# Performance work log

Hardware: AMD Instinct MI355X
Metric: run time of the kernel (lower is better)

The kernel has to match this reference:

```python
import jax, jax.numpy as jnp
import numpy as np

D_MODEL = 1024
H = 16
D_K = D_MODEL // H


def setup_inputs() -> dict:
    key = jax.random.key(0)
    ks = jax.random.split(key, 9)
    s = 0.02
    x = jax.random.normal(ks[0], (2, 2048, D_MODEL), dtype=jnp.float32)
    Wq = jax.random.normal(ks[1], (D_MODEL, D_MODEL), dtype=jnp.float32) * s
    bq = jax.random.normal(ks[2], (D_MODEL,), dtype=jnp.float32) * s
    Wk = jax.random.normal(ks[3], (D_MODEL, D_MODEL), dtype=jnp.float32) * s
    bk = jax.random.normal(ks[4], (D_MODEL,), dtype=jnp.float32) * s
    Wv = jax.random.normal(ks[5], (D_MODEL, D_MODEL), dtype=jnp.float32) * s
    bv = jax.random.normal(ks[6], (D_MODEL,), dtype=jnp.float32) * s
    Wo = jax.random.normal(ks[7], (D_MODEL, D_MODEL), dtype=jnp.float32) * s
    bo = jax.random.normal(ks[8], (D_MODEL,), dtype=jnp.float32) * s
    return {"x": x, "Wq": Wq, "bq": bq, "Wk": Wk, "bk": bk,
            "Wv": Wv, "bv": bv, "Wo": Wo, "bo": bo}


def reference(x, Wq, bq, Wk, bk, Wv, bv, Wo, bo):
    b, s, _ = x.shape
    scale = 1.0 / jnp.sqrt(jnp.float32(D_K))
    # projections; [b, s, d] -> [b, h, s, d_k]
    def split_heads(t):
        return t.reshape(b, s, H, D_K).transpose(0, 2, 1, 3)
    q = split_heads(x @ Wq + bq)
    k = split_heads(x @ Wk + bk)
    v = split_heads(x @ Wv + bv)
    scores = jnp.einsum('bhqd,bhkd->bhqk', q, k) * scale  # [b,h,s,s]
    attn = jax.nn.softmax(scores, axis=-1)
    ctx = jnp.einsum('bhqk,bhkd->bhqd', attn, v)
    ctx = ctx.transpose(0, 2, 1, 3).reshape(b, s, D_MODEL)
    return ctx @ Wo + bo + x
```

## Files before the change

### kernel.cpp

```cpp
#include <hip/hip_runtime.h>
#include <hip/hip_bf16.h>
#include <stdint.h>

#define D_MODEL 1024
#define NH 16
#define DK 64
#define S_LEN 2048

typedef __attribute__((ext_vector_type(8))) __bf16 bf16x8;
typedef __attribute__((ext_vector_type(4))) float f32x4;

#define GLOBAL_AS __attribute__((address_space(1)))
#define LDS_AS    __attribute__((address_space(3)))

__device__ __forceinline__ void async16(const ushort* g, ushort* l) {
    __builtin_amdgcn_global_load_lds(
        (const GLOBAL_AS uint32_t*)(uintptr_t)(const void*)g,
        (LDS_AS uint32_t*)(uint32_t)(uintptr_t)(void*)l,
        16, 0, 0);
}

template <int N>
__device__ __forceinline__ void pipe_barrier() {
    asm volatile("s_waitcnt vmcnt(%0)\n\ts_barrier" :: "n"(N) : "memory");
}

__device__ __forceinline__ float fast_exp2(float x) {
    float r;
    asm("v_exp_f32 %0, %1" : "=v"(r) : "v"(x));
    return r;
}

__device__ __forceinline__ ushort f2bf(float f) {
    union { float f; uint32_t u; } v; v.f = f;
    uint32_t lsb = (v.u >> 16) & 1u;
    return (ushort)((v.u + 0x7fffu + lsb) >> 16);
}

__device__ __forceinline__ uint32_t packbf(float a, float b) {
    union { float f; uint32_t u; } x, y; x.f = a; y.f = b;
    return ((x.u + 0x8000u) >> 16) | ((y.u + 0x8000u) & 0xffff0000u);
}

__device__ __forceinline__ uint32_t packbf_rn(float a, float b) {
    union { __hip_bfloat162 h; uint32_t u; } cv;
    cv.h = __float22bfloat162_rn(make_float2(a, b));
    return cv.u;
}

__device__ __forceinline__ bf16x8 ldfrag(const ushort* p) {
    union { uint4 u; bf16x8 b; } cv;
    cv.u = *(const uint4*)p;
    return cv.b;
}


__global__ void cvt_x_kernel(const float* __restrict__ x, ushort* __restrict__ xb) {
    int i = blockIdx.x * 256 + threadIdx.x;
    float4 v = ((const float4*)x)[i];
    ushort4 o;
    o.x = f2bf(v.x); o.y = f2bf(v.y); o.z = f2bf(v.z); o.w = f2bf(v.w);
    ((ushort4*)xb)[i] = o;
}

__global__ void transpose_cvt4_kernel(
    const float* __restrict__ W0, const float* __restrict__ W1,
    const float* __restrict__ W2, const float* __restrict__ W3,
    ushort* __restrict__ D0, ushort* __restrict__ D1,
    ushort* __restrict__ D2, ushort* __restrict__ D3) {
    const float* W; ushort* D;
    switch (blockIdx.z) {
        case 0: W = W0; D = D0; break;
        case 1: W = W1; D = D1; break;
        case 2: W = W2; D = D2; break;
        default: W = W3; D = D3; break;
    }
    __shared__ float tile[32][33];
    int bx = blockIdx.x * 32, by = blockIdx.y * 32;
    int tx = threadIdx.x, ty = threadIdx.y;
#pragma unroll
    for (int j = 0; j < 32; j += 8)
        tile[ty + j][tx] = W[(size_t)(by + ty + j) * D_MODEL + bx + tx];
    __syncthreads();
#pragma unroll
    for (int j = 0; j < 32; j += 8)
        D[(size_t)(bx + ty + j) * D_MODEL + by + tx] = f2bf(tile[tx][ty + j]);
}

__global__ void cvt_bias_kernel(const float* __restrict__ bq, const float* __restrict__ bk,
                                const float* __restrict__ bv, float* __restrict__ out) {
    int i = blockIdx.x * 256 + threadIdx.x;
    float v = (i < 1024) ? bq[i] : (i < 2048 ? bk[i - 1024] : bv[i - 2048]);
    out[i] = v;
}

template <int MODE>
__global__ __launch_bounds__(256, 3) void gemm_kernel(
    const ushort* __restrict__ A, const ushort* __restrict__ Bt,
    const float* __restrict__ bias,
    ushort* __restrict__ outQ, ushort* __restrict__ outK, ushort* __restrict__ outVt,
    const float* __restrict__ xres, float* __restrict__ outF) {
    constexpr int BN = (MODE == 0) ? 128 : 64;
    constexpr int NI = (MODE == 0) ? 4 : 2;
    constexpr int NS = (MODE == 0) ? 4 : 3;
    constexpr int ABUF = 4096;
    constexpr int BBUF = (MODE == 0) ? 4096 : 2048;
    constexpr int SMEM = (MODE == 0) ? 24576 : 18432;
    __shared__ __align__(16) ushort smem[SMEM];
    ushort* sAb = smem;
    ushort* sBb = smem + 3 * ABUF;

    const int tid = threadIdx.x;
    const int wave = tid >> 6, lane = tid & 63;
    const int lr = lane & 15, lq = lane >> 4;
    const int srow = lane >> 3, sp = lane & 7;

    const int bid = blockIdx.x;
    const int xcd = bid & 7, lb = bid >> 3;
    int bx, by;
    if (MODE == 0) { bx = xcd * 3 + (lb % 3); by = lb / 3; }
    else           { by = xcd * 4 + (lb & 3); bx = lb >> 2; }
    const int blockM = by * 128;
    const int blockN = bx * BN;
    const int waveM = (wave >> 1) * 64;
    const int waveN = (MODE == 0) ? (wave & 1) * 64 : (wave & 1) * 32;

    auto stage = [&](int k0, int buf) {
        ushort* a = sAb + buf * ABUF;
#pragma unroll
        for (int t = 0; t < 2; t++) {
            int Rb = wave * 16 + t * 8;
            int R = Rb + srow;
            int L = sp ^ (R & 7);
            int m = 2 * R + (L >> 2);
            int kc = L & 3;
            async16(&A[(size_t)(blockM + m) * D_MODEL + k0 + kc * 8], a + Rb * 64);
        }
        ushort* b = sBb + buf * BBUF;
        if (MODE == 0) {
#pragma unroll
            for (int t = 0; t < 2; t++) {
                int Rb = wave * 16 + t * 8;
                int R = Rb + srow;
                int L = sp ^ (R & 7);
                int n = 2 * R + (L >> 2);
                int kc = L & 3;
                async16(&Bt[(size_t)(blockN + n) * D_MODEL + k0 + kc * 8], b + Rb * 64);
            }
        } else {
            int Rb = wave * 8;
            int R = Rb + srow;
            int L = sp ^ (R & 7);
            int n = 2 * R + (L >> 2);
            int kc = L & 3;
            async16(&Bt[(size_t)(blockN + n) * D_MODEL + k0 + kc * 8], b + Rb * 64);
        }
    };

    const int RA = (waveM >> 1) + (lr >> 1);
    const int offA = RA * 64 + ((((lr & 1) * 4 + lq) ^ (RA & 7)) * 8);
    const int RB = (waveN >> 1) + (lr >> 1);
    const int offB = RB * 64 + ((((lr & 1) * 4 + lq) ^ (RB & 7)) * 8);

    f32x4 acc[4][NI] = {};

    stage(0, 0);
    stage(32, 1);
    pipe_barrier<NS>();

#pragma unroll
    for (int k = 0; k < 32; k++) {
        const int buf = k % 3;
        if (k + 2 < 32) stage((k + 2) * 32, (k + 2) % 3);
        const ushort* a = sAb + buf * ABUF;
        const ushort* b = sBb + buf * BBUF;
        bf16x8 af[4], bfr[NI];
#pragma unroll
        for (int mi = 0; mi < 4; mi++)
            af[mi] = ldfrag(&a[offA + mi * 512]);
#pragma unroll
        for (int ni = 0; ni < NI; ni++)
            bfr[ni] = ldfrag(&b[offB + ni * 512]);
#pragma unroll
        for (int mi = 0; mi < 4; mi++)
#pragma unroll
            for (int ni = 0; ni < NI; ni++)
                acc[mi][ni] = __builtin_amdgcn_mfma_f32_16x16x32_bf16(
                    af[mi], bfr[ni], acc[mi][ni], 0, 0, 0);
        if (k < 30) pipe_barrier<NS>();
        else if (k == 30) pipe_barrier<0>();
    }
    __syncthreads();

    const int bglob = blockM >> 11;
    const int sbase = blockM & 2047;

    if (MODE == 0) {
        const int which = bx >> 3;
        if (which < 2) {
            const float scale = (which == 0) ? 0.1803368801f : 1.0f;
#pragma unroll
            for (int ni = 0; ni < 4; ni++) {
                const int n_loc = waveN + ni * 16 + lr;
                const float bn = bias[blockN + n_loc];
#pragma unroll
                for (int mi = 0; mi < 4; mi++)
#pragma unroll
                    for (int r = 0; r < 4; r++) {
                        int m_loc = waveM + mi * 16 + lq * 4 + r;
                        smem[m_loc * 136 + n_loc] =
                            f2bf((acc[mi][ni][r] + bn) * scale);
                    }
            }
            __syncthreads();
            ushort* outp = (which == 0) ? outQ : outK;
            const int hbase = (which == 0) ? bx * 2 : (bx - 8) * 2;
#pragma unroll
            for (int j = 0; j < 8; j++) {
                int c = tid + j * 256;
                int m = c >> 4, nc = c & 15;
                int hh = nc >> 3, d8 = nc & 7;
                uint4 w = *(uint4*)&smem[m * 136 + nc * 8];
                size_t bh = (size_t)(bglob * NH + hbase + hh);
                *(uint4*)&outp[(bh * S_LEN + sbase + m) * DK + d8 * 8] = w;
            }
        } else {
#pragma unroll
            for (int ni = 0; ni < 4; ni++) {
                const int n_loc = waveN + ni * 16 + lr;
                const float bn = bias[blockN + n_loc];
#pragma unroll
                for (int mi = 0; mi < 4; mi++) {
                    uint2 w;
                    w.x = packbf(acc[mi][ni][0] + bn, acc[mi][ni][1] + bn);
                    w.y = packbf(acc[mi][ni][2] + bn, acc[mi][ni][3] + bn);
                    int m_base = waveM + mi * 16 + lq * 4;
                    *(uint2*)&smem[n_loc * 136 + m_base] = w;
                }
            }
            __syncthreads();
            const int hbase = (bx - 16) * 2;
#pragma unroll
            for (int j = 0; j < 8; j++) {
                int c = tid + j * 256;
                int n_loc = c >> 4, m8 = c & 15;
                int d = n_loc & 63, hh = n_loc >> 6;
                uint4 w = *(uint4*)&smem[n_loc * 136 + m8 * 8];
                size_t bh = (size_t)(bglob * NH + hbase + hh);
                *(uint4*)&outVt[(bh * DK + d) * S_LEN + sbase + m8 * 8] = w;
            }
        }
    } else {
        float* sCf = (float*)smem;
#pragma unroll
        for (int ni = 0; ni < 2; ni++) {
            const int n_loc = waveN + ni * 16 + lr;
            const float bn = bias[blockN + n_loc];
#pragma unroll
            for (int mi = 0; mi < 4; mi++)
#pragma unroll
                for (int r = 0; r < 4; r++) {
                    int m_loc = waveM + mi * 16 + lq * 4 + r;
                    sCf[m_loc * 68 + n_loc] = acc[mi][ni][r] + bn;
                }
        }
        __syncthreads();
#pragma unroll
        for (int j = 0; j < 8; j++) {
            int c = tid + j * 256;
            int m = c >> 4, nc = c & 15;
            float4 v = *(float4*)&sCf[m * 68 + nc * 4];
            size_t idx = (size_t)(blockM + m) * D_MODEL + blockN + nc * 4;
            float4 xr = *(const float4*)&xres[idx];
            v.x += xr.x; v.y += xr.y; v.z += xr.z; v.w += xr.w;
            *(float4*)&outF[idx] = v;
        }
    }
}

__global__ __launch_bounds__(256, 3) void attn_kernel(
    const ushort* __restrict__ Q, const ushort* __restrict__ Km,
    const ushort* __restrict__ Vt, ushort* __restrict__ ctx) {
    const int bid = blockIdx.x;
    const int xcd = bid & 7, lb = bid >> 3;
    const int bh = xcd * 4 + (lb & 3);
    const int qt = lb >> 2;
    const int q0 = qt * 128;
    __shared__ __align__(16) ushort sK[2][64 * 64];
    __shared__ __align__(16) ushort sV[2][64 * 64];
    __shared__ __align__(16) ushort sQP[4][32 * 64];
    const int tid = threadIdx.x;
    const int wave = tid >> 6, lane = tid & 63;
    const int lr = lane & 15, lq = lane >> 4;
    const int srow = lane >> 3, sp = lane & 7;
    const ushort* Qh = Q + (size_t)bh * S_LEN * DK;
    const ushort* Kh = Km + (size_t)bh * S_LEN * DK;
    const ushort* Vh = Vt + (size_t)bh * DK * S_LEN;
    ushort* sPw = sQP[wave];

#pragma unroll
    for (int t = 0; t < 4; t++) {
        int row = t * 8 + srow;
        int c = sp ^ (row & 7);
        async16(&Qh[(size_t)(q0 + wave * 32 + row) * DK + c * 8],
                &sPw[t * 8 * 64]);
    }

    auto stageK = [&](int k0, int buf) {
#pragma unroll
        for (int t = 0; t < 2; t++) {
            int row = wave * 16 + t * 8 + srow;
            int c = sp ^ (row & 7);
            async16(&Kh[(size_t)(k0 + row) * DK + c * 8],
                    &sK[buf][(wave * 16 + t * 8) * 64]);
        }
    };
    auto stageV = [&](int k0, int buf) {
#pragma unroll
        for (int t = 0; t < 2; t++) {
            int row = wave * 16 + t * 8 + srow;
            int c = sp ^ (row & 7);
            async16(&Vh[(size_t)row * S_LEN + k0 + c * 8],
                    &sV[buf][(wave * 16 + t * 8) * 64]);
        }
    };

    stageK(0, 0);
    stageV(0, 0);
    stageK(64, 1);
    __syncthreads();

    bf16x8 qf[2][2];
#pragma unroll
    for (int nj = 0; nj < 2; nj++)
#pragma unroll
        for (int kk = 0; kk < 2; kk++)
            qf[nj][kk] = ldfrag(&sPw[(nj * 16 + lr) * 64 +
                                     (((kk * 4 + lq) ^ (lr & 7)) * 8)]);

    union { uint4 u; bf16x8 b; } one_u;
    one_u.u = make_uint4(0x3F803F80u, 0x3F803F80u, 0x3F803F80u, 0x3F803F80u);
    const bf16x8 ones = one_u.b;

    f32x4 cacc[2][4] = {};
    f32x4 ssum[2] = {};

    auto qk = [&](const ushort* sk, f32x4 (*sacc)[2]) {
#pragma unroll
        for (int kk = 0; kk < 2; kk++) {
            bf16x8 kf[4];
            int swz = ((kk * 4 + lq) ^ (lr & 7)) * 8;
#pragma unroll
            for (int mi = 0; mi < 4; mi++)
                kf[mi] = ldfrag(&sk[(mi * 16 + lr) * 64 + swz]);
            __builtin_amdgcn_s_setprio(1);
#pragma unroll
            for (int mi = 0; mi < 4; mi++)
#pragma unroll
                for (int nj = 0; nj < 2; nj++)
                    sacc[mi][nj] = __builtin_amdgcn_mfma_f32_16x16x32_bf16(
                        kf[mi], qf[nj][kk], sacc[mi][nj], 0, 0, 0);
            __builtin_amdgcn_s_setprio(0);
        }
    };

    auto expP = [&](f32x4 (*sacc)[2]) {
#pragma unroll
        for (int mi = 0; mi < 4; mi++)
#pragma unroll
            for (int nj = 0; nj < 2; nj++) {
                float p0 = fast_exp2(sacc[mi][nj][0]);
                float p1 = fast_exp2(sacc[mi][nj][1]);
                float p2 = fast_exp2(sacc[mi][nj][2]);
                float p3 = fast_exp2(sacc[mi][nj][3]);
                uint2 w;
                w.x = packbf_rn(p0, p1);
                w.y = packbf_rn(p2, p3);
                int physc = (mi * 2 + (lq >> 1)) ^ (lr & 7);
                *(uint2*)&sPw[(nj * 16 + lr) * 64 + physc * 8 + (lq & 1) * 4] = w;
            }
    };

    auto pv = [&](const ushort* sv) {
#pragma unroll
        for (int ks = 0; ks < 2; ks++) {
            bf16x8 pf[2], vf[4];
            int swz = ((ks * 4 + lq) ^ (lr & 7)) * 8;
#pragma unroll
            for (int nj = 0; nj < 2; nj++)
                pf[nj] = ldfrag(&sPw[(nj * 16 + lr) * 64 + swz]);
#pragma unroll
            for (int nd = 0; nd < 4; nd++)
                vf[nd] = ldfrag(&sv[(nd * 16 + lr) * 64 + swz]);
            __builtin_amdgcn_s_setprio(1);
#pragma unroll
            for (int nj = 0; nj < 2; nj++)
#pragma unroll
                for (int nd = 0; nd < 4; nd++)
                    cacc[nj][nd] = __builtin_amdgcn_mfma_f32_16x16x32_bf16(
                        pf[nj], vf[nd], cacc[nj][nd], 0, 0, 0);
#pragma unroll
            for (int nj = 0; nj < 2; nj++)
                ssum[nj] = __builtin_amdgcn_mfma_f32_16x16x32_bf16(
                    pf[nj], ones, ssum[nj], 0, 0, 0);
            __builtin_amdgcn_s_setprio(0);
        }
    };

    {
        f32x4 s0[4][2] = {};
        qk(sK[0], s0);
        expP(s0);
    }
    __builtin_amdgcn_s_barrier();

#pragma unroll 2
    for (int k = 0; k < 31; k++) {
        if (k + 2 < 32) stageK((k + 2) * 64, k & 1);
        stageV((k + 1) * 64, (k + 1) & 1);
        f32x4 s2[4][2] = {};
        qk(sK[(k + 1) & 1], s2);
        pv(sV[k & 1]);
        pipe_barrier<0>();
        expP(s2);
    }
    pv(sV[1]);

    const int b = bh >> 4, h = bh & 15;
    float inv[2][4];
#pragma unroll
    for (int nj = 0; nj < 2; nj++)
#pragma unroll
        for (int r = 0; r < 4; r++)
            inv[nj][r] = __builtin_amdgcn_rcpf(ssum[nj][r]);
#pragma unroll
    for (int nj = 0; nj < 2; nj++)
#pragma unroll
        for (int nd = 0; nd < 4; nd++)
#pragma unroll
            for (int r = 0; r < 4; r++) {
                int qrow = q0 + wave * 32 + nj * 16 + lq * 4 + r;
                int d = nd * 16 + lr;
                float v = cacc[nj][nd][r] * inv[nj][r];
                ctx[(size_t)(b * S_LEN + qrow) * D_MODEL + h * DK + d] = f2bf(v);
            }
}


extern "C" void kernel_launch(void* const* d_in, const int* in_sizes, int n_in,
                              void* d_out, int out_size, void* d_ws, size_t ws_size,
                              hipStream_t stream) {
    const float* x  = (const float*)d_in[0];
    const float* Wq = (const float*)d_in[1];
    const float* bq = (const float*)d_in[2];
    const float* Wk = (const float*)d_in[3];
    const float* bk = (const float*)d_in[4];
    const float* Wv = (const float*)d_in[5];
    const float* bv = (const float*)d_in[6];
    const float* Wo = (const float*)d_in[7];
    const float* bo = (const float*)d_in[8];

    char* ws = (char*)d_ws;
    ushort* xb    = (ushort*)(ws);
    ushort* wqkv  = (ushort*)(ws + (8ull  << 20));
    ushort* wo_t  = (ushort*)(ws + (14ull << 20));
    ushort* qbuf  = (ushort*)(ws + (16ull << 20));
    ushort* kbuf  = (ushort*)(ws + (24ull << 20));
    ushort* vtb   = (ushort*)(ws + (32ull << 20));
    ushort* ctx   = (ushort*)(ws + (40ull << 20));
    float*  biasq = (float*)(ws + (48ull << 20));

    cvt_x_kernel<<<4096, 256, 0, stream>>>(x, xb);
    transpose_cvt4_kernel<<<dim3(32, 32, 4), dim3(32, 8), 0, stream>>>(
        Wq, Wk, Wv, Wo, wqkv, wqkv + 1024 * 1024, wqkv + 2 * 1024 * 1024, wo_t);
    cvt_bias_kernel<<<12, 256, 0, stream>>>(bq, bk, bv, biasq);

    gemm_kernel<0><<<768, 256, 0, stream>>>(
        xb, wqkv, biasq, qbuf, kbuf, vtb, nullptr, nullptr);
    attn_kernel<<<512, 256, 0, stream>>>(qbuf, kbuf, vtb, ctx);
    gemm_kernel<1><<<512, 256, 0, stream>>>(
        ctx, wo_t, bo, nullptr, nullptr, nullptr, x, (float*)d_out);
}
```

Measured before the change: 188.5 us.

## Triple-buffer K/V in attention and fuse the three conversion kernels into one launch

The attention kernel moves from double to triple buffering of the K and V LDS tiles. It prefetches one tile further ahead and waits on a partial vmcnt instead of draining all loads each iteration, so global loads overlap more with MFMA work. LDS use grows and launch bounds drop from 3 to 2 blocks per CU, which may lower occupancy. Separately, the x-cast, weight-transpose and bias-copy kernels are merged into a single launch to save two kernel launches.

```diff
diff --git a/kernel.cpp b/kernel.cpp
--- a/kernel.cpp
+++ b/kernel.cpp
@@ -54,44 +54,46 @@
     return cv.b;
 }
 
-
-__global__ void cvt_x_kernel(const float* __restrict__ x, ushort* __restrict__ xb) {
-    int i = blockIdx.x * 256 + threadIdx.x;
-    float4 v = ((const float4*)x)[i];
-    ushort4 o;
-    o.x = f2bf(v.x); o.y = f2bf(v.y); o.z = f2bf(v.z); o.w = f2bf(v.w);
-    ((ushort4*)xb)[i] = o;
-}
-
-__global__ void transpose_cvt4_kernel(
+__global__ void cvt_fused_kernel(
+    const float* __restrict__ x, ushort* __restrict__ xb,
     const float* __restrict__ W0, const float* __restrict__ W1,
     const float* __restrict__ W2, const float* __restrict__ W3,
     ushort* __restrict__ D0, ushort* __restrict__ D1,
-    ushort* __restrict__ D2, ushort* __restrict__ D3) {
-    const float* W; ushort* D;
-    switch (blockIdx.z) {
-        case 0: W = W0; D = D0; break;
-        case 1: W = W1; D = D1; break;
-        case 2: W = W2; D = D2; break;
-        default: W = W3; D = D3; break;
-    }
+    ushort* __restrict__ D2, ushort* __restrict__ D3,
+    const float* __restrict__ bq, const float* __restrict__ bk,
+    const float* __restrict__ bv, float* __restrict__ biasq) {
     __shared__ float tile[32][33];
-    int bx = blockIdx.x * 32, by = blockIdx.y * 32;
-    int tx = threadIdx.x, ty = threadIdx.y;
-#pragma unroll
-    for (int j = 0; j < 32; j += 8)
-        tile[ty + j][tx] = W[(size_t)(by + ty + j) * D_MODEL + bx + tx];
-    __syncthreads();
-#pragma unroll
-    for (int j = 0; j < 32; j += 8)
-        D[(size_t)(bx + ty + j) * D_MODEL + by + tx] = f2bf(tile[tx][ty + j]);
-}
-
-__global__ void cvt_bias_kernel(const float* __restrict__ bq, const float* __restrict__ bk,
-                                const float* __restrict__ bv, float* __restrict__ out) {
-    int i = blockIdx.x * 256 + threadIdx.x;
-    float v = (i < 1024) ? bq[i] : (i < 2048 ? bk[i - 1024] : bv[i - 2048]);
-    out[i] = v;
+    const int bid = blockIdx.x, tid = threadIdx.x;
+    if (bid < 4096) {
+        int i = bid * 256 + tid;
+        float4 v = ((const float4*)x)[i];
+        ushort4 o;
+        o.x = f2bf(v.x); o.y = f2bf(v.y); o.z = f2bf(v.z); o.w = f2bf(v.w);
+        ((ushort4*)xb)[i] = o;
+    } else if (bid < 8192) {
+        int t = bid - 4096;
+        int z = t >> 10, rem = t & 1023;
+        const float* W; ushort* D;
+        switch (z) {
+            case 0: W = W0; D = D0; break;
+            case 1: W = W1; D = D1; break;
+            case 2: W = W2; D = D2; break;
+            default: W = W3; D = D3; break;
+        }
+        int by = (rem >> 5) * 32, bx = (rem & 31) * 32;
+        int tx = tid & 31, ty = tid >> 5;
+#pragma unroll
+        for (int j = 0; j < 32; j += 8)
+            tile[ty + j][tx] = W[(size_t)(by + ty + j) * D_MODEL + bx + tx];
+        __syncthreads();
+#pragma unroll
+        for (int j = 0; j < 32; j += 8)
+            D[(size_t)(bx + ty + j) * D_MODEL + by + tx] = f2bf(tile[tx][ty + j]);
+    } else {
+        int i = (bid - 8192) * 256 + tid;
+        float v = (i < 1024) ? bq[i] : (i < 2048 ? bk[i - 1024] : bv[i - 2048]);
+        biasq[i] = v;
+    }
 }
 
 template <int MODE>
@@ -278,7 +280,7 @@
     }
 }
 
-__global__ __launch_bounds__(256, 3) void attn_kernel(
+__global__ __launch_bounds__(256, 2) void attn_kernel(
     const ushort* __restrict__ Q, const ushort* __restrict__ Km,
     const ushort* __restrict__ Vt, ushort* __restrict__ ctx) {
     const int bid = blockIdx.x;
@@ -286,8 +288,8 @@
     const int bh = xcd * 4 + (lb & 3);
     const int qt = lb >> 2;
     const int q0 = qt * 128;
-    __shared__ __align__(16) ushort sK[2][64 * 64];
-    __shared__ __align__(16) ushort sV[2][64 * 64];
+    __shared__ __align__(16) ushort sK[3][64 * 64];
+    __shared__ __align__(16) ushort sV[3][64 * 64];
     __shared__ __align__(16) ushort sQP[4][32 * 64];
     const int tid = threadIdx.x;
     const int wave = tid >> 6, lane = tid & 63;
@@ -328,6 +330,8 @@
     stageK(0, 0);
     stageV(0, 0);
     stageK(64, 1);
+    stageV(64, 1);
+    stageK(128, 2);
     __syncthreads();
 
     bf16x8 qf[2][2];
@@ -414,17 +418,19 @@
     }
     __builtin_amdgcn_s_barrier();
 
-#pragma unroll 2
+#pragma unroll 3
     for (int k = 0; k < 31; k++) {
-        if (k + 2 < 32) stageK((k + 2) * 64, k & 1);
-        stageV((k + 1) * 64, (k + 1) & 1);
+        if (k + 3 < 32) stageK((k + 3) * 64, (k + 3) % 3);
+        if (k + 2 < 32) stageV((k + 2) * 64, (k + 2) % 3);
         f32x4 s2[4][2] = {};
-        qk(sK[(k + 1) & 1], s2);
-        pv(sV[k & 1]);
-        pipe_barrier<0>();
+        qk(sK[(k + 1) % 3], s2);
+        pv(sV[k % 3]);
+        if (k < 29) pipe_barrier<4>();
+        else if (k == 29) pipe_barrier<2>();
+        else pipe_barrier<0>();
         expP(s2);
     }
-    pv(sV[1]);
+    pv(sV[31 % 3]);
 
     const int b = bh >> 4, h = bh & 15;
     float inv[2][4];
@@ -470,10 +476,10 @@
     ushort* ctx   = (ushort*)(ws + (40ull << 20));
     float*  biasq = (float*)(ws + (48ull << 20));
 
-    cvt_x_kernel<<<4096, 256, 0, stream>>>(x, xb);
-    transpose_cvt4_kernel<<<dim3(32, 32, 4), dim3(32, 8), 0, stream>>>(
-        Wq, Wk, Wv, Wo, wqkv, wqkv + 1024 * 1024, wqkv + 2 * 1024 * 1024, wo_t);
-    cvt_bias_kernel<<<12, 256, 0, stream>>>(bq, bk, bv, biasq);
+    cvt_fused_kernel<<<8204, 256, 0, stream>>>(
+        x, xb, Wq, Wk, Wv, Wo,
+        wqkv, wqkv + 1024 * 1024, wqkv + 2 * 1024 * 1024, wo_t,
+        bq, bk, bv, biasq);
 
     gemm_kernel<0><<<768, 256, 0, stream>>>(
         xb, wqkv, biasq, qbuf, kbuf, vtb, nullptr, nullptr);
```

New measurement: 186.7 us, median of 3. Within noise of the previous version (-0.9%).

## Fuse all stages into one persistent kernel with grid-wide barriers

Applied to the files above, without the earlier changes.

Replaces the six separate launches (conversions, QKV GEMM, attention, output GEMM) with one persistent 768-block kernel that runs each phase in turn, separated by atomic-counter grid barriers. Shared memory is unified into one buffer reused by each phase. The goal is to remove per-launch overhead and the gaps between kernels. In exchange it relies on all 768 blocks being co-resident (256 CUs times 3 blocks), which would deadlock otherwise. Barrier spinning adds cost, and during attention and the output GEMM only 512 of the 768 blocks do work.

```diff
diff --git a/kernel.cpp b/kernel.cpp
--- a/kernel.cpp
+++ b/kernel.cpp
@@ -6,6 +6,7 @@
 #define NH 16
 #define DK 64
 #define S_LEN 2048
+#define GRID_N 768u
 
 typedef __attribute__((ext_vector_type(8))) __bf16 bf16x8;
 typedef __attribute__((ext_vector_type(4))) float f32x4;
@@ -54,48 +55,24 @@
     return cv.b;
 }
 
-
-__global__ void cvt_x_kernel(const float* __restrict__ x, ushort* __restrict__ xb) {
-    int i = blockIdx.x * 256 + threadIdx.x;
-    float4 v = ((const float4*)x)[i];
-    ushort4 o;
-    o.x = f2bf(v.x); o.y = f2bf(v.y); o.z = f2bf(v.z); o.w = f2bf(v.w);
-    ((ushort4*)xb)[i] = o;
-}
-
-__global__ void transpose_cvt4_kernel(
-    const float* __restrict__ W0, const float* __restrict__ W1,
-    const float* __restrict__ W2, const float* __restrict__ W3,
-    ushort* __restrict__ D0, ushort* __restrict__ D1,
-    ushort* __restrict__ D2, ushort* __restrict__ D3) {
-    const float* W; ushort* D;
-    switch (blockIdx.z) {
-        case 0: W = W0; D = D0; break;
-        case 1: W = W1; D = D1; break;
-        case 2: W = W2; D = D2; break;
-        default: W = W3; D = D3; break;
-    }
-    __shared__ float tile[32][33];
-    int bx = blockIdx.x * 32, by = blockIdx.y * 32;
-    int tx = threadIdx.x, ty = threadIdx.y;
-#pragma unroll
-    for (int j = 0; j < 32; j += 8)
-        tile[ty + j][tx] = W[(size_t)(by + ty + j) * D_MODEL + bx + tx];
+__device__ __forceinline__ void grid_bar(uint32_t* cnt) {
     __syncthreads();
-#pragma unroll
-    for (int j = 0; j < 32; j += 8)
-        D[(size_t)(bx + ty + j) * D_MODEL + by + tx] = f2bf(tile[tx][ty + j]);
-}
-
-__global__ void cvt_bias_kernel(const float* __restrict__ bq, const float* __restrict__ bk,
-                                const float* __restrict__ bv, float* __restrict__ out) {
-    int i = blockIdx.x * 256 + threadIdx.x;
-    float v = (i < 1024) ? bq[i] : (i < 2048 ? bk[i - 1024] : bv[i - 2048]);
-    out[i] = v;
+    if (threadIdx.x == 0) {
+        __threadfence();
+        uint32_t ticket = __hip_atomic_fetch_add(
+            cnt, 1u, __ATOMIC_ACQ_REL, __HIP_MEMORY_SCOPE_AGENT);
+        uint32_t target = (ticket / GRID_N + 1u) * GRID_N;
+        while (__hip_atomic_load(cnt, __ATOMIC_ACQUIRE,
+                                 __HIP_MEMORY_SCOPE_AGENT) < target)
+            __builtin_amdgcn_s_sleep(16);
+        __threadfence();
+    }
+    __syncthreads();
 }
 
 template <int MODE>
-__global__ __launch_bounds__(256, 3) void gemm_kernel(
+__device__ __forceinline__ void gemm_body(
+    int bid, ushort* smem,
     const ushort* __restrict__ A, const ushort* __restrict__ Bt,
     const float* __restrict__ bias,
     ushort* __restrict__ outQ, ushort* __restrict__ outK, ushort* __restrict__ outVt,
@@ -105,8 +82,6 @@
     constexpr int NS = (MODE == 0) ? 4 : 3;
     constexpr int ABUF = 4096;
     constexpr int BBUF = (MODE == 0) ? 4096 : 2048;
-    constexpr int SMEM = (MODE == 0) ? 24576 : 18432;
-    __shared__ __align__(16) ushort smem[SMEM];
     ushort* sAb = smem;
     ushort* sBb = smem + 3 * ABUF;
 
@@ -115,7 +90,6 @@
     const int lr = lane & 15, lq = lane >> 4;
     const int srow = lane >> 3, sp = lane & 7;
 
-    const int bid = blockIdx.x;
     const int xcd = bid & 7, lb = bid >> 3;
     int bx, by;
     if (MODE == 0) { bx = xcd * 3 + (lb % 3); by = lb / 3; }
@@ -278,17 +252,17 @@
     }
 }
 
-__global__ __launch_bounds__(256, 3) void attn_kernel(
+__device__ __forceinline__ void attn_body(
+    int bid, ushort* smem,
     const ushort* __restrict__ Q, const ushort* __restrict__ Km,
     const ushort* __restrict__ Vt, ushort* __restrict__ ctx) {
-    const int bid = blockIdx.x;
     const int xcd = bid & 7, lb = bid >> 3;
     const int bh = xcd * 4 + (lb & 3);
     const int qt = lb >> 2;
     const int q0 = qt * 128;
-    __shared__ __align__(16) ushort sK[2][64 * 64];
-    __shared__ __align__(16) ushort sV[2][64 * 64];
-    __shared__ __align__(16) ushort sQP[4][32 * 64];
+    ushort* sKb = smem;
+    ushort* sVb = smem + 8192;
+    ushort* sQP = smem + 16384;
     const int tid = threadIdx.x;
     const int wave = tid >> 6, lane = tid & 63;
     const int lr = lane & 15, lq = lane >> 4;
@@ -296,7 +270,7 @@
     const ushort* Qh = Q + (size_t)bh * S_LEN * DK;
     const ushort* Kh = Km + (size_t)bh * S_LEN * DK;
     const ushort* Vh = Vt + (size_t)bh * DK * S_LEN;
-    ushort* sPw = sQP[wave];
+    ushort* sPw = sQP + wave * 2048;
 
 #pragma unroll
     for (int t = 0; t < 4; t++) {
@@ -312,7 +286,7 @@
             int row = wave * 16 + t * 8 + srow;
             int c = sp ^ (row & 7);
             async16(&Kh[(size_t)(k0 + row) * DK + c * 8],
-                    &sK[buf][(wave * 16 + t * 8) * 64]);
+                    sKb + buf * 4096 + (wave * 16 + t * 8) * 64);
         }
     };
     auto stageV = [&](int k0, int buf) {
@@ -321,7 +295,7 @@
             int row = wave * 16 + t * 8 + srow;
             int c = sp ^ (row & 7);
             async16(&Vh[(size_t)row * S_LEN + k0 + c * 8],
-                    &sV[buf][(wave * 16 + t * 8) * 64]);
+                    sVb + buf * 4096 + (wave * 16 + t * 8) * 64);
         }
     };
 
@@ -409,7 +383,7 @@
 
     {
         f32x4 s0[4][2] = {};
-        qk(sK[0], s0);
+        qk(sKb, s0);
         expP(s0);
     }
     __builtin_amdgcn_s_barrier();
@@ -419,12 +393,12 @@
         if (k + 2 < 32) stageK((k + 2) * 64, k & 1);
         stageV((k + 1) * 64, (k + 1) & 1);
         f32x4 s2[4][2] = {};
-        qk(sK[(k + 1) & 1], s2);
-        pv(sV[k & 1]);
+        qk(sKb + ((k + 1) & 1) * 4096, s2);
+        pv(sVb + (k & 1) * 4096);
         pipe_barrier<0>();
         expP(s2);
     }
-    pv(sV[1]);
+    pv(sVb + 4096);
 
     const int b = bh >> 4, h = bh & 15;
     float inv[2][4];
@@ -444,6 +418,78 @@
                 float v = cacc[nj][nd][r] * inv[nj][r];
                 ctx[(size_t)(b * S_LEN + qrow) * D_MODEL + h * DK + d] = f2bf(v);
             }
+}
+
+__global__ __launch_bounds__(256, 3) void mega_kernel(
+    const float* __restrict__ x,
+    const float* __restrict__ Wq, const float* __restrict__ bq,
+    const float* __restrict__ Wk, const float* __restrict__ bk,
+    const float* __restrict__ Wv, const float* __restrict__ bv,
+    const float* __restrict__ Wo, const float* __restrict__ bo,
+    char* __restrict__ ws, float* __restrict__ outF) {
+    __shared__ __align__(16) ushort smem[24576];
+
+    ushort* xb    = (ushort*)(ws);
+    ushort* wqkv  = (ushort*)(ws + (8ull  << 20));
+    ushort* wo_t  = (ushort*)(ws + (14ull << 20));
+    ushort* qbuf  = (ushort*)(ws + (16ull << 20));
+    ushort* kbuf  = (ushort*)(ws + (24ull << 20));
+    ushort* vtb   = (ushort*)(ws + (32ull << 20));
+    ushort* ctxb  = (ushort*)(ws + (40ull << 20));
+    float*  biasq = (float*)(ws + (48ull << 20));
+    uint32_t* bar = (uint32_t*)(ws + (49ull << 20));
+
+    const int tid = threadIdx.x;
+
+    for (int wb = blockIdx.x; wb < 8204; wb += 768) {
+        if (wb < 4096) {
+            int i = wb * 256 + tid;
+            float4 v = ((const float4*)x)[i];
+            ushort4 o;
+            o.x = f2bf(v.x); o.y = f2bf(v.y); o.z = f2bf(v.z); o.w = f2bf(v.w);
+            ((ushort4*)xb)[i] = o;
+        } else if (wb < 8192) {
+            float (*tile)[33] = (float(*)[33])(void*)smem;
+            int t = wb - 4096;
+            int z = t >> 10, rem = t & 1023;
+            const float* W; ushort* D;
+            switch (z) {
+                case 0: W = Wq; D = wqkv; break;
+                case 1: W = Wk; D = wqkv + 1024 * 1024; break;
+                case 2: W = Wv; D = wqkv + 2 * 1024 * 1024; break;
+                default: W = Wo; D = wo_t; break;
+            }
+            int by = (rem >> 5) * 32, bx = (rem & 31) * 32;
+            int tx = tid & 31, ty = tid >> 5;
+#pragma unroll
+            for (int j = 0; j < 32; j += 8)
+                tile[ty + j][tx] = W[(size_t)(by + ty + j) * D_MODEL + bx + tx];
+            __syncthreads();
+#pragma unroll
+            for (int j = 0; j < 32; j += 8)
+                D[(size_t)(bx + ty + j) * D_MODEL + by + tx] =
+                    f2bf(tile[tx][ty + j]);
+            __syncthreads();
+        } else {
+            int i = (wb - 8192) * 256 + tid;
+            float v = (i < 1024) ? bq[i]
+                                 : (i < 2048 ? bk[i - 1024] : bv[i - 2048]);
+            biasq[i] = v;
+        }
+    }
+    grid_bar(bar);
+
+    gemm_body<0>(blockIdx.x, smem, xb, wqkv, biasq,
+                 qbuf, kbuf, vtb, nullptr, nullptr);
+    grid_bar(bar);
+
+    if (blockIdx.x < 512)
+        attn_body(blockIdx.x, smem, qbuf, kbuf, vtb, ctxb);
+    grid_bar(bar);
+
+    if (blockIdx.x < 512)
+        gemm_body<1>(blockIdx.x, smem, ctxb, wo_t, bo,
+                     nullptr, nullptr, nullptr, x, outF);
 }
 
 
@@ -459,25 +505,11 @@
     const float* bv = (const float*)d_in[6];
     const float* Wo = (const float*)d_in[7];
     const float* bo = (const float*)d_in[8];
-
     char* ws = (char*)d_ws;
-    ushort* xb    = (ushort*)(ws);
-    ushort* wqkv  = (ushort*)(ws + (8ull  << 20));
-    ushort* wo_t  = (ushort*)(ws + (14ull << 20));
-    ushort* qbuf  = (ushort*)(ws + (16ull << 20));
-    ushort* kbuf  = (ushort*)(ws + (24ull << 20));
-    ushort* vtb   = (ushort*)(ws + (32ull << 20));
-    ushort* ctx   = (ushort*)(ws + (40ull << 20));
-    float*  biasq = (float*)(ws + (48ull << 20));
-
-    cvt_x_kernel<<<4096, 256, 0, stream>>>(x, xb);
-    transpose_cvt4_kernel<<<dim3(32, 32, 4), dim3(32, 8), 0, stream>>>(
-        Wq, Wk, Wv, Wo, wqkv, wqkv + 1024 * 1024, wqkv + 2 * 1024 * 1024, wo_t);
-    cvt_bias_kernel<<<12, 256, 0, stream>>>(bq, bk, bv, biasq);
-
-    gemm_kernel<0><<<768, 256, 0, stream>>>(
-        xb, wqkv, biasq, qbuf, kbuf, vtb, nullptr, nullptr);
-    attn_kernel<<<512, 256, 0, stream>>>(qbuf, kbuf, vtb, ctx);
-    gemm_kernel<1><<<512, 256, 0, stream>>>(
-        ctx, wo_t, bo, nullptr, nullptr, nullptr, x, (float*)d_out);
-}
+    float* outF = (float*)d_out;
+
+    hipMemsetAsync(ws + (49ull << 20), 0, 4, stream);
+
+    mega_kernel<<<768, 256, 0, stream>>>(
+        x, Wq, bq, Wk, bk, Wv, bv, Wo, bo, ws, outF);
+}
```

Result: slower. 609.9 us (+223.7%).
